# Kernel optimization log

Measured on AMD Instinct MI355X. Metric: run time of the kernel, lower is better.

## Reference

```python
import jax, jax.numpy as jnp
import numpy as np

K = 16  # nsample


def _conv2d(x, w, b=None):
    # 1x1 conv2d: x [B,Cin,K,N], w [Cout,Cin]
    y = jnp.einsum('oc,bckn->bokn', w, x)
    return y if b is None else y + b[None, :, None, None]


def setup_inputs() -> dict:
    key = jax.random.key(0)
    ks = jax.random.split(key, 20)
    B, N1, N2, C = 2, 4096, 8192, 64
    Cin = C + 3  # in_channel + 3
    w = lambda k, shape, fan: (jax.random.normal(k, shape, jnp.float32) / np.sqrt(fan).astype(np.float32))
    return {
        'xyz1': jax.random.normal(ks[0], (B, 3, N1), jnp.float32),
        'xyz2': jax.random.normal(ks[1], (B, 3, N2), jnp.float32),
        'points1': jax.random.normal(ks[2], (B, C, N1), jnp.float32),
        'points2': jax.random.normal(ks[3], (B, C, N2), jnp.float32),
        'w_r0': w(ks[4], (C, Cin), Cin), 'b_r0': jnp.zeros((C,), jnp.float32),
        'w_r1': w(ks[5], (C, C), C), 'b_r1': jnp.zeros((C,), jnp.float32),
        'w_z0': w(ks[6], (C, Cin), Cin), 'b_z0': jnp.zeros((C,), jnp.float32),
        'w_z1': w(ks[7], (C, C), C), 'b_z1': jnp.zeros((C,), jnp.float32),
        'w_h0': w(ks[8], (C, Cin), Cin), 'b_h0': jnp.zeros((C,), jnp.float32),
        'w_h1': w(ks[9], (C, C), C), 'b_h1': jnp.zeros((C,), jnp.float32),
        'w_fuse_r': w(ks[10], (C, C), C),
        'w_fuse_z': w(ks[11], (C, C), C),
        'w_fuse_ro': w(ks[12], (C, C), C),
    }


def reference(xyz1, xyz2, points1, points2,
              w_r0, b_r0, w_r1, b_r1,
              w_z0, b_z0, w_z1, b_z1,
              w_h0, b_h0, w_h1, b_h1,
              w_fuse_r, w_fuse_z, w_fuse_ro):
    x1 = jnp.transpose(xyz1, (0, 2, 1))  # [B,N1,3]
    x2 = jnp.transpose(xyz2, (0, 2, 1))  # [B,N2,3]
    # squared pairwise distances [B,N1,N2]
    sq = (jnp.sum(x1 * x1, -1)[:, :, None]
          + jnp.sum(x2 * x2, -1)[:, None, :]
          - 2.0 * jnp.einsum('bnd,bmd->bnm', x1, x2))
    _, knn = jax.lax.top_k(-sq, K)  # [B,N1,K] smallest distances
    gather = jax.vmap(lambda p, i: p[i])
    nbr_xyz = gather(x2, knn)                 # [B,N1,K,3]
    dir_xyz = nbr_xyz - x1[:, :, None, :]
    p2 = gather(jnp.transpose(points2, (0, 2, 1)), knn)  # [B,N1,K,C]
    new_pts = jnp.transpose(jnp.concatenate([p2, dir_xyz], -1), (0, 3, 2, 1))  # [B,C+3,K,N1]

    lrelu = lambda v: jax.nn.leaky_relu(v, 0.1)
    fuse = lambda w, p: jnp.einsum('oc,bcn->bon', w, p)

    # r gate
    r = _conv2d(new_pts, w_r0, b_r0) + fuse(w_fuse_r, points1)[:, :, None, :]
    r = lrelu(r)
    r = jax.nn.sigmoid(_conv2d(r, w_r1, b_r1))  # [B,C,K,N1]

    # z gate (max over neighbors before last conv)
    z = _conv2d(new_pts, w_z0, b_z0) + fuse(w_fuse_z, points1)[:, :, None, :]
    z = lrelu(z)
    z = jnp.max(z, axis=2, keepdims=True)
    z = jax.nn.sigmoid(_conv2d(z, w_z1, b_z1))[:, :, 0, :]  # [B,C,N1]

    # h candidate
    p1e = _conv2d(r * points1[:, :, None, :], w_fuse_ro)
    h = lrelu(_conv2d(new_pts, w_h0, b_h0) + p1e)
    h = jnp.max(h, axis=2, keepdims=True)
    h = jnp.tanh(_conv2d(h, w_h1, b_h1))[:, :, 0, :]  # [B,C,N1]

    return (1.0 - z) * points1 + z * h
```

## Files before the change

### kernel.cpp

```cpp
#include <hip/hip_runtime.h>
#include <math.h>

typedef __attribute__((ext_vector_type(8))) short bf8_t;
typedef __attribute__((ext_vector_type(4))) float f32x4;

#define NB   2
#define N1S  4096
#define N2S  8192
#define CC   64
#define KK   16
#define GQ   8
#define KTILE 2048

#define M_R0 0
#define M_Z0 1
#define M_H0 2
#define M_R1 3
#define M_Z1 4
#define M_H1 5
#define M_FR 6
#define M_FZ 7
#define M_FRO 8

#define WA_SHORTS   (9*4*2*64*8)
#define WDIR_OFF    (WA_SHORTS*2)
#define WDIR_FLOATS (3*3*64)
#define XP_OFF      (WDIR_OFF + WDIR_FLOATS*4)
#define XP_BYTES    (NB*N2S*16)
#define KIDX_OFF    (XP_OFF + XP_BYTES)
#define KIDX_BYTES  (NB*N1S*KK*4)
#define P2B_OFF     (KIDX_OFF + KIDX_BYTES)
#define P2B_BYTES   ((size_t)NB*N2S*CC*2)

__device__ __forceinline__ float lrelu(float v){ return v > 0.f ? v : 0.1f*v; }
__device__ __forceinline__ float sigm(float v){ return 1.f/(1.f + __expf(-v)); }
__device__ __forceinline__ float tanh_(float v){ return 1.f - 2.f/(__expf(2.f*v) + 1.f); }
__device__ __forceinline__ unsigned short f2bf(float f){
  union { float f; unsigned u; } v; v.f = f;
  unsigned r = v.u + 0x7FFF + ((v.u >> 16) & 1);
  return (unsigned short)(r >> 16);
}

__global__ __launch_bounds__(256) void prep_wA(
    const float* __restrict__ r0, const float* __restrict__ z0, const float* __restrict__ h0,
    const float* __restrict__ r1, const float* __restrict__ z1, const float* __restrict__ h1,
    const float* __restrict__ fr, const float* __restrict__ fz, const float* __restrict__ fro,
    short* __restrict__ wa, float* __restrict__ wdir)
{
  const float* W[9] = {r0, z0, h0, r1, z1, h1, fr, fz, fro};
  const int Ks[9]   = {67, 67, 67, 64, 64, 64, 64, 64, 64};
  const int stride = gridDim.x * 256;
  for (int i = blockIdx.x*256 + threadIdx.x; i < WA_SHORTS; i += stride) {
    const int j = i & 7, l = (i >> 3) & 63, kk = (i >> 9) & 1, r = (i >> 10) & 3, mat = i >> 12;
    const int row = r*16 + (l & 15);
    const int c = kk*32 + ((l >> 4) << 3) + j;
    wa[i] = (short)f2bf(W[mat][row*Ks[mat] + c]);
  }
  for (int i = blockIdx.x*256 + threadIdx.x; i < WDIR_FLOATS; i += stride) {
    const int g = i / 192, rem = i % 192, d = rem / 64, o = rem & 63;
    wdir[i] = W[g][o*67 + 64 + d];
  }
}

__global__ __launch_bounds__(256) void pack_xyz2(const float* __restrict__ xyz2, float4* __restrict__ xp){
  const int i = blockIdx.x*256 + threadIdx.x;
  const int b = i >> 13, j = i & (N2S-1);
  const float x = xyz2[((size_t)(b*3+0))*N2S + j];
  const float y = xyz2[((size_t)(b*3+1))*N2S + j];
  const float z = xyz2[((size_t)(b*3+2))*N2S + j];
  xp[i] = make_float4(x, y, z, (x*x + y*y) + z*z);
}

__global__ __launch_bounds__(256) void transpose_p2(const float* __restrict__ src, unsigned short* __restrict__ dst){
  __shared__ float t[64][65];
  const int b = blockIdx.y; const int j0 = blockIdx.x*64;
  const int tx = threadIdx.x & 63; const int r4 = threadIdx.x >> 6;
  #pragma unroll
  for (int c = r4; c < 64; c += 4) t[c][tx] = src[((size_t)b*CC + c)*N2S + j0 + tx];
  __syncthreads();
  #pragma unroll
  for (int j = r4; j < 64; j += 4) dst[((size_t)b*N2S + j0 + j)*CC + tx] = f2bf(t[tx][j]);
}

__global__ __launch_bounds__(256) void knn_kernel(
    const float* __restrict__ xyz1, const float4* __restrict__ xp, int* __restrict__ idxout)
{
  __shared__ float4 T[KTILE];
  const int tid = threadIdx.x, w = tid >> 6, lane = tid & 63, grp = lane >> 4;
  const int qbase = blockIdx.x*16 + w*4;
  const int b = qbase >> 12;
  const float4* __restrict__ X = xp + (b << 13);
  float qx[4], qy[4], qz[4], s1[4], kth[4], kappa[4], m[4];
  #pragma unroll
  for (int g = 0; g < 4; g++) {
    const int n = (qbase + g) & (N1S-1);
    qx[g] = xyz1[((size_t)(b*3+0))*N1S + n];
    qy[g] = xyz1[((size_t)(b*3+1))*N1S + n];
    qz[g] = xyz1[((size_t)(b*3+2))*N1S + n];
    s1[g] = (qx[g]*qx[g] + qy[g]*qy[g]) + qz[g]*qz[g];
    kth[g] = INFINITY; m[g] = INFINITY;
  }

  #pragma unroll 2
  for (int c0 = 0; c0 < N2S; c0 += 256) {
    const float4 v0 = X[c0 + lane];
    const float4 v1 = X[c0 + 64 + lane];
    const float4 v2 = X[c0 + 128 + lane];
    const float4 v3 = X[c0 + 192 + lane];
    #pragma unroll
    for (int g = 0; g < 4; g++) {
      const float d0 = (s1[g] + v0.w) - 2.f*((qx[g]*v0.x + qy[g]*v0.y) + qz[g]*v0.z);
      const float d1 = (s1[g] + v1.w) - 2.f*((qx[g]*v1.x + qy[g]*v1.y) + qz[g]*v1.z);
      const float d2 = (s1[g] + v2.w) - 2.f*((qx[g]*v2.x + qy[g]*v2.y) + qz[g]*v2.z);
      const float d3 = (s1[g] + v3.w) - 2.f*((qx[g]*v3.x + qy[g]*v3.y) + qz[g]*v3.z);
      m[g] = fminf(m[g], fminf(fminf(d0, d1), fminf(d2, d3)));
    }
  }
  #pragma unroll
  for (int g = 0; g < 4; g++) {
    float v = m[g];
    #pragma unroll
    for (int k = 2; k <= 64; k <<= 1) {
      #pragma unroll
      for (int j = k >> 1; j > 0; j >>= 1) {
        const float pv = __shfl_xor(v, j);
        const bool up = ((lane & k) == 0);
        const bool keepmin = up ? ((lane & j) == 0) : ((lane & j) != 0);
        v = keepmin ? fminf(v, pv) : fmaxf(v, pv);
      }
    }
    kappa[g] = __shfl(v, 16);
  }

  float listd = INFINITY; int listi = 0;
  for (int t0 = 0; t0 < N2S; t0 += KTILE) {
    __syncthreads();
    for (int i = tid; i < KTILE; i += 256) T[i] = X[t0 + i];
    __syncthreads();
    for (int c0 = 0; c0 < KTILE; c0 += 64) {
      const float4 v = T[c0 + lane];
      #pragma unroll
      for (int g = 0; g < 4; g++) {
        const float d = (s1[g] + v.w) - 2.f*((qx[g]*v.x + qy[g]*v.y) + qz[g]*v.z);
        unsigned long long vote = __ballot(d < fminf(kth[g], kappa[g]));
        while (vote) {
          const int src = (int)__builtin_ctzll(vote);
          vote &= vote - 1;
          const float dv = __shfl(d, src);
          if (dv < kth[g]) {
            const int iv = t0 + c0 + src;
            const float ud = __shfl_up(listd, 1);
            const int   ui = __shfl_up(listi, 1);
            const bool ing = (grp == g);
            const bool cm = ing && (dv < listd);
            const bool cp = cm && ((lane & 15) > 0) && (dv < ud);
            listd = cm ? (cp ? ud : dv) : listd;
            listi = cm ? (cp ? ui : iv) : listi;
            kth[g] = __shfl(listd, g*16 + 15);
          }
        }
      }
    }
  }

  {
    bool need = false;
    #pragma unroll
    for (int g = 0; g < 4; g++) need = need || (kth[g] == INFINITY);
    if (__builtin_expect(need, 0)) {
      #pragma unroll
      for (int g = 0; g < 4; g++) {
        if (kth[g] == INFINITY) {
          if (grp == g) { listd = INFINITY; listi = 0; }
          float kk2 = INFINITY;
          for (int c0 = 0; c0 < N2S; c0 += 64) {
            const float4 v = X[c0 + lane];
            const float d = (s1[g] + v.w) - 2.f*((qx[g]*v.x + qy[g]*v.y) + qz[g]*v.z);
            unsigned long long vote = __ballot(d < kk2);
            while (vote) {
              const int src = (int)__builtin_ctzll(vote);
              vote &= vote - 1;
              const float dv = __shfl(d, src);
              if (dv < kk2) {
                const int iv = c0 + src;
                const float ud = __shfl_up(listd, 1);
                const int   ui = __shfl_up(listi, 1);
                const bool ing = (grp == g);
                const bool cm = ing && (dv < listd);
                const bool cp = cm && ((lane & 15) > 0) && (dv < ud);
                listd = cm ? (cp ? ud : dv) : listd;
                listi = cm ? (cp ? ui : iv) : listi;
                kk2 = __shfl(listd, g*16 + 15);
              }
            }
          }
        }
      }
    }
  }
  idxout[(size_t)(qbase + grp)*KK + (lane & 15)] = listi;
}

#define FRAG(mat, kk) (*(const bf8_t*)(wA + (((mat)*4 + w)*2 + (kk))*512 + lane*8))

__global__ __launch_bounds__(256) void gates_kernel(
    const float* __restrict__ xyz1, const float* __restrict__ xyz2,
    const float* __restrict__ points1, const unsigned short* __restrict__ p2b,
    const int* __restrict__ kidx, const short* __restrict__ wA,
    const float* __restrict__ wdir,
    const float* __restrict__ b_r0, const float* __restrict__ b_z0,
    const float* __restrict__ b_h0, const float* __restrict__ b_r1,
    const float* __restrict__ b_z1, const float* __restrict__ b_h1,
    float* __restrict__ out)
{
  __shared__ __align__(16) short featB[2][GQ][64][8];
  __shared__ __align__(16) short rB[2][GQ][64][8];
  __shared__ __align__(16) float p1f[64][GQ];
  __shared__ __align__(16) short p1B[2][64][8];
  __shared__ float BFr[64][GQ], BFz[64][GQ];
  __shared__ float zmaxL[64][GQ], hmaxL[64][GQ];
  __shared__ float biasL[6][64];
  __shared__ float dirL[3][GQ*KK];
  __shared__ __align__(16) float obuf[64][GQ];

  const int tid = threadIdx.x;
  const int w = tid >> 6, lane = tid & 63;
  const int b  = blockIdx.x >> 9;
  const int n0 = (blockIdx.x & 511) * GQ;
  const int cq = lane & 15;
  const int reg_o0 = w*16 + ((lane >> 4) << 2);
  const f32x4 zero4 = {0.f, 0.f, 0.f, 0.f};

  for (int i = tid; i < 6*64; i += 256) {
    const int a = i >> 6, o = i & 63;
    const float* bp = (a==0)?b_r0:(a==1)?b_z0:(a==2)?b_h0:(a==3)?b_r1:(a==4)?b_z1:b_h1;
    biasL[a][o] = bp[o];
  }
  if (tid < 64) {
    const float* sp = points1 + ((size_t)(b*CC + tid))*N1S + n0;
    *(float4*)&p1f[tid][0] = ((const float4*)sp)[0];
    *(float4*)&p1f[tid][4] = ((const float4*)sp)[1];
  }
  ((unsigned long long*)&p1B[0][0][0])[tid] = 0ULL;
  if (tid < 128) {
    const int m = tid, qg = n0 + (m >> 4);
    const int j = kidx[(size_t)((b << 12) + qg)*KK + (m & 15)];
    #pragma unroll
    for (int d = 0; d < 3; d++)
      dirL[d][m] = xyz2[((size_t)(b*3+d))*N2S + j] - xyz1[((size_t)(b*3+d))*N1S + qg];
  }
  {
    const int m = tid >> 1, half = tid & 1;
    const int ct = m >> 4;
    const int qg = n0 + ct;
    const int j = kidx[(size_t)((b << 12) + qg)*KK + (m & 15)];
    const uint4* __restrict__ src = (const uint4*)(p2b + (((size_t)(b << 13) + j)*CC + half*32));
    #pragma unroll
    for (int gi = 0; gi < 4; gi++)
      *(uint4*)&featB[half][ct][gi*16 + (m & 15)][0] = src[gi];
  }
  __syncthreads();

  {
    const int s0 = tid*4;
    const int j0 = s0 & 7, l = (s0 >> 3) & 63, kk = s0 >> 9;
    const int q = l & 15;
    if (q < 8) {
      unsigned short t0[4];
      #pragma unroll
      for (int jj = 0; jj < 4; jj++)
        t0[jj] = f2bf(p1f[kk*32 + ((l >> 4) << 3) + j0 + jj][q]);
      uint2 pk; pk.x = t0[0] | ((unsigned)t0[1] << 16); pk.y = t0[2] | ((unsigned)t0[3] << 16);
      *(uint2*)&p1B[kk][l][j0] = pk;
    }
  }
  __syncthreads();

  {
    const bf8_t fa0 = FRAG(M_FR, 0), fa1 = FRAG(M_FR, 1);
    const bf8_t ga0 = FRAG(M_FZ, 0), ga1 = FRAG(M_FZ, 1);
    const bf8_t pb0 = *(const bf8_t*)&p1B[0][lane][0];
    const bf8_t pb1 = *(const bf8_t*)&p1B[1][lane][0];
    f32x4 ar = __builtin_amdgcn_mfma_f32_16x16x32_bf16(fa0, pb0, zero4, 0, 0, 0);
    ar = __builtin_amdgcn_mfma_f32_16x16x32_bf16(fa1, pb1, ar, 0, 0, 0);
    f32x4 az = __builtin_amdgcn_mfma_f32_16x16x32_bf16(ga0, pb0, zero4, 0, 0, 0);
    az = __builtin_amdgcn_mfma_f32_16x16x32_bf16(ga1, pb1, az, 0, 0, 0);
    if (cq < 8) {
      #pragma unroll
      for (int r2 = 0; r2 < 4; r2++) {
        const int o = reg_o0 + r2;
        BFr[o][cq] = ar[r2] + biasL[0][o];
        BFz[o][cq] = az[r2] + biasL[1][o];
      }
    }
  }

  {
    const bf8_t ra0 = FRAG(M_R0, 0), ra1 = FRAG(M_R0, 1);
    const bf8_t za0 = FRAG(M_Z0, 0), za1 = FRAG(M_Z0, 1);
    float wdr[3][4], wdz[3][4];
    #pragma unroll
    for (int d = 0; d < 3; d++)
      #pragma unroll
      for (int r2 = 0; r2 < 4; r2++) {
        wdr[d][r2] = wdir[(0*3 + d)*64 + reg_o0 + r2];
        wdz[d][r2] = wdir[(1*3 + d)*64 + reg_o0 + r2];
      }
    const int kkv = reg_o0 >> 5, lp = ((reg_o0 & 31) >> 3)*16 + cq, j0 = reg_o0 & 7;
    #pragma unroll
    for (int ct = 0; ct < GQ; ct++) {
      const bf8_t fb0 = *(const bf8_t*)&featB[0][ct][lane][0];
      const bf8_t fb1 = *(const bf8_t*)&featB[1][ct][lane][0];
      f32x4 accr = __builtin_amdgcn_mfma_f32_16x16x32_bf16(ra0, fb0, zero4, 0, 0, 0);
      accr = __builtin_amdgcn_mfma_f32_16x16x32_bf16(ra1, fb1, accr, 0, 0, 0);
      f32x4 accz = __builtin_amdgcn_mfma_f32_16x16x32_bf16(za0, fb0, zero4, 0, 0, 0);
      accz = __builtin_amdgcn_mfma_f32_16x16x32_bf16(za1, fb1, accz, 0, 0, 0);
      const int m = ct*16 + cq;
      const float d0 = dirL[0][m], d1 = dirL[1][m], d2 = dirL[2][m];
      unsigned short rpk[4]; float zv[4];
      #pragma unroll
      for (int r2 = 0; r2 < 4; r2++) {
        const int o = reg_o0 + r2;
        float rv = accr[r2] + BFr[o][ct] + wdr[0][r2]*d0 + wdr[1][r2]*d1 + wdr[2][r2]*d2;
        rpk[r2] = f2bf(lrelu(rv));
        float zt = accz[r2] + BFz[o][ct] + wdz[0][r2]*d0 + wdz[1][r2]*d1 + wdz[2][r2]*d2;
        zv[r2] = lrelu(zt);
      }
      uint2 pk; pk.x = rpk[0] | ((unsigned)rpk[1] << 16); pk.y = rpk[2] | ((unsigned)rpk[3] << 16);
      *(uint2*)&rB[kkv][ct][lp][j0] = pk;
      #pragma unroll
      for (int r2 = 0; r2 < 4; r2++) {
        float vv = zv[r2];
        vv = fmaxf(vv, __shfl_xor(vv, 1));
        vv = fmaxf(vv, __shfl_xor(vv, 2));
        vv = fmaxf(vv, __shfl_xor(vv, 4));
        vv = fmaxf(vv, __shfl_xor(vv, 8));
        zv[r2] = vv;
      }
      if (cq == 0) {
        #pragma unroll
        for (int r2 = 0; r2 < 4; r2++) zmaxL[reg_o0 + r2][ct] = zv[r2];
      }
    }
  }
  __syncthreads();

  uint2 rpK[GQ];
  float zg[4];
  {
    const bf8_t r1a0 = FRAG(M_R1, 0), r1a1 = FRAG(M_R1, 1);
    #pragma unroll
    for (int ct = 0; ct < GQ; ct++) {
      const bf8_t b0 = *(const bf8_t*)&rB[0][ct][lane][0];
      const bf8_t b1 = *(const bf8_t*)&rB[1][ct][lane][0];
      f32x4 acc = __builtin_amdgcn_mfma_f32_16x16x32_bf16(r1a0, b0, zero4, 0, 0, 0);
      acc = __builtin_amdgcn_mfma_f32_16x16x32_bf16(r1a1, b1, acc, 0, 0, 0);
      unsigned short pk4[4];
      #pragma unroll
      for (int r2 = 0; r2 < 4; r2++) {
        const int o = reg_o0 + r2;
        const float rg = sigm(acc[r2] + biasL[3][o]);
        pk4[r2] = f2bf(rg * p1f[o][ct]);
      }
      rpK[ct].x = pk4[0] | ((unsigned)pk4[1] << 16);
      rpK[ct].y = pk4[2] | ((unsigned)pk4[3] << 16);
    }
    const bf8_t z1a0 = FRAG(M_Z1, 0), z1a1 = FRAG(M_Z1, 1);
    const int qc = cq < 8 ? cq : 7;
    bf8_t zb0, zb1;
    #pragma unroll
    for (int j = 0; j < 8; j++) {
      zb0[j] = (short)f2bf(zmaxL[((lane >> 4) << 3) + j][qc]);
      zb1[j] = (short)f2bf(zmaxL[32 + ((lane >> 4) << 3) + j][qc]);
    }
    f32x4 az = __builtin_amdgcn_mfma_f32_16x16x32_bf16(z1a0, zb0, zero4, 0, 0, 0);
    az = __builtin_amdgcn_mfma_f32_16x16x32_bf16(z1a1, zb1, az, 0, 0, 0);
    #pragma unroll
    for (int r2 = 0; r2 < 4; r2++) zg[r2] = sigm(az[r2] + biasL[4][reg_o0 + r2]);
  }
  __syncthreads();

  {
    const int kkv = reg_o0 >> 5, lp = ((reg_o0 & 31) >> 3)*16 + cq, j0 = reg_o0 & 7;
    #pragma unroll
    for (int ct = 0; ct < GQ; ct++) *(uint2*)&rB[kkv][ct][lp][j0] = rpK[ct];
  }
  __syncthreads();

  {
    const bf8_t h0a0 = FRAG(M_H0, 0), h0a1 = FRAG(M_H0, 1);
    const bf8_t foa0 = FRAG(M_FRO, 0), foa1 = FRAG(M_FRO, 1);
    float wdh[3][4];
    #pragma unroll
    for (int d = 0; d < 3; d++)
      #pragma unroll
      for (int r2 = 0; r2 < 4; r2++) wdh[d][r2] = wdir[(2*3 + d)*64 + reg_o0 + r2];
    #pragma unroll
    for (int ct = 0; ct < GQ; ct++) {
      const bf8_t fb0 = *(const bf8_t*)&featB[0][ct][lane][0];
      const bf8_t fb1 = *(const bf8_t*)&featB[1][ct][lane][0];
      const bf8_t rb0 = *(const bf8_t*)&rB[0][ct][lane][0];
      const bf8_t rb1 = *(const bf8_t*)&rB[1][ct][lane][0];
      f32x4 acc = __builtin_amdgcn_mfma_f32_16x16x32_bf16(h0a0, fb0, zero4, 0, 0, 0);
      acc = __builtin_amdgcn_mfma_f32_16x16x32_bf16(h0a1, fb1, acc, 0, 0, 0);
      acc = __builtin_amdgcn_mfma_f32_16x16x32_bf16(foa0, rb0, acc, 0, 0, 0);
      acc = __builtin_amdgcn_mfma_f32_16x16x32_bf16(foa1, rb1, acc, 0, 0, 0);
      const int m = ct*16 + cq;
      const float d0 = dirL[0][m], d1 = dirL[1][m], d2 = dirL[2][m];
      float hv[4];
      #pragma unroll
      for (int r2 = 0; r2 < 4; r2++) {
        const int o = reg_o0 + r2;
        hv[r2] = lrelu(acc[r2] + biasL[2][o] + wdh[0][r2]*d0 + wdh[1][r2]*d1 + wdh[2][r2]*d2);
      }
      #pragma unroll
      for (int r2 = 0; r2 < 4; r2++) {
        float vv = hv[r2];
        vv = fmaxf(vv, __shfl_xor(vv, 1));
        vv = fmaxf(vv, __shfl_xor(vv, 2));
        vv = fmaxf(vv, __shfl_xor(vv, 4));
        vv = fmaxf(vv, __shfl_xor(vv, 8));
        hv[r2] = vv;
      }
      if (cq == 0) {
        #pragma unroll
        for (int r2 = 0; r2 < 4; r2++) hmaxL[reg_o0 + r2][ct] = hv[r2];
      }
    }
  }
  __syncthreads();

  {
    const bf8_t h1a0 = FRAG(M_H1, 0), h1a1 = FRAG(M_H1, 1);
    const int qc = cq < 8 ? cq : 7;
    bf8_t hb0, hb1;
    #pragma unroll
    for (int j = 0; j < 8; j++) {
      hb0[j] = (short)f2bf(hmaxL[((lane >> 4) << 3) + j][qc]);
      hb1[j] = (short)f2bf(hmaxL[32 + ((lane >> 4) << 3) + j][qc]);
    }
    f32x4 ah = __builtin_amdgcn_mfma_f32_16x16x32_bf16(h1a0, hb0, zero4, 0, 0, 0);
    ah = __builtin_amdgcn_mfma_f32_16x16x32_bf16(h1a1, hb1, ah, 0, 0, 0);
    if (cq < 8) {
      #pragma unroll
      for (int r2 = 0; r2 < 4; r2++) {
        const int o = reg_o0 + r2;
        const float hg = tanh_(ah[r2] + biasL[5][o]);
        obuf[o][cq] = (1.f - zg[r2])*p1f[o][cq] + zg[r2]*hg;
      }
    }
  }
  __syncthreads();
  if (tid < 128) {
    const int c = tid >> 1, q4 = (tid & 1)*4;
    *(float4*)(out + ((size_t)(b*CC + c))*N1S + n0 + q4) = *(float4*)&obuf[c][q4];
  }
}

extern "C" void kernel_launch(void* const* d_in, const int* in_sizes, int n_in,
                              void* d_out, int out_size, void* d_ws, size_t ws_size,
                              hipStream_t stream) {
  const float* xyz1    = (const float*)d_in[0];
  const float* xyz2    = (const float*)d_in[1];
  const float* points1 = (const float*)d_in[2];
  const float* points2 = (const float*)d_in[3];
  const float* w_r0 = (const float*)d_in[4];
  const float* b_r0 = (const float*)d_in[5];
  const float* w_r1 = (const float*)d_in[6];
  const float* b_r1 = (const float*)d_in[7];
  const float* w_z0 = (const float*)d_in[8];
  const float* b_z0 = (const float*)d_in[9];
  const float* w_z1 = (const float*)d_in[10];
  const float* b_z1 = (const float*)d_in[11];
  const float* w_h0 = (const float*)d_in[12];
  const float* b_h0 = (const float*)d_in[13];
  const float* w_h1 = (const float*)d_in[14];
  const float* b_h1 = (const float*)d_in[15];
  const float* w_fr  = (const float*)d_in[16];
  const float* w_fz  = (const float*)d_in[17];
  const float* w_fro = (const float*)d_in[18];
  float* out = (float*)d_out;

  short*  wa   = (short*)d_ws;
  float*  wdir = (float*)((char*)d_ws + WDIR_OFF);
  float4* xp   = (float4*)((char*)d_ws + XP_OFF);
  int*    kidx = (int*)((char*)d_ws + KIDX_OFF);
  unsigned short* p2b = (unsigned short*)((char*)d_ws + P2B_OFF);

  prep_wA<<<16, 256, 0, stream>>>(w_r0, w_z0, w_h0, w_r1, w_z1, w_h1,
                                  w_fr, w_fz, w_fro, wa, wdir);
  pack_xyz2<<<64, 256, 0, stream>>>(xyz2, xp);
  transpose_p2<<<dim3(N2S/64, NB), dim3(256), 0, stream>>>(points2, p2b);

  knn_kernel<<<512, 256, 0, stream>>>(xyz1, xp, kidx);

  gates_kernel<<<1024, 256, 0, stream>>>(
      xyz1, xyz2, points1, p2b, kidx, wa, wdir,
      b_r0, b_z0, b_h0, b_r1, b_z1, b_h1, out);
}
```

Baseline: 202.8 us.

## Split KNN candidate scan across two waves per query and merge lists

The KNN kernel now gives each wave 2 queries instead of 4 and splits the 8192 candidates into two halves handled by paired waves. The per-half top-16 lists are merged through shared memory with a bitonic sort that breaks ties by index. The LDS tile staging of candidates is dropped, and the scan reads global memory directly. This quadruples the block count to raise parallelism and occupancy, and shortens the serial per-wave scan. In exchange it adds a merge step and pays for twice the kappa prefilter work over the halves.

Measured after the change: 199.2 us. No clear change (-1.8%).

```diff
diff --git a/kernel.cpp b/kernel.cpp
--- a/kernel.cpp
+++ b/kernel.cpp
@@ -10,7 +10,6 @@
 #define CC   64
 #define KK   16
 #define GQ   8
-#define KTILE 2048
 
 #define M_R0 0
 #define M_Z0 1
@@ -85,15 +84,19 @@
 __global__ __launch_bounds__(256) void knn_kernel(
     const float* __restrict__ xyz1, const float4* __restrict__ xp, int* __restrict__ idxout)
 {
-  __shared__ float4 T[KTILE];
+  __shared__ float pdL[4][2][16];
+  __shared__ int   piL[4][2][16];
   const int tid = threadIdx.x, w = tid >> 6, lane = tid & 63, grp = lane >> 4;
-  const int qbase = blockIdx.x*16 + w*4;
+  const int qbase = blockIdx.x*4;
   const int b = qbase >> 12;
+  const int q0 = qbase + (w >> 1)*2;
+  const int half = w & 1;
+  const int hbase = half*(N2S/2);
   const float4* __restrict__ X = xp + (b << 13);
-  float qx[4], qy[4], qz[4], s1[4], kth[4], kappa[4], m[4];
+  float qx[2], qy[2], qz[2], s1[2], kth[2], kappa[2], m[2];
   #pragma unroll
-  for (int g = 0; g < 4; g++) {
-    const int n = (qbase + g) & (N1S-1);
+  for (int g = 0; g < 2; g++) {
+    const int n = (q0 + g) & (N1S-1);
     qx[g] = xyz1[((size_t)(b*3+0))*N1S + n];
     qy[g] = xyz1[((size_t)(b*3+1))*N1S + n];
     qz[g] = xyz1[((size_t)(b*3+2))*N1S + n];
@@ -102,13 +105,13 @@
   }
 
   #pragma unroll 2
-  for (int c0 = 0; c0 < N2S; c0 += 256) {
-    const float4 v0 = X[c0 + lane];
-    const float4 v1 = X[c0 + 64 + lane];
-    const float4 v2 = X[c0 + 128 + lane];
-    const float4 v3 = X[c0 + 192 + lane];
-    #pragma unroll
-    for (int g = 0; g < 4; g++) {
+  for (int c0 = 0; c0 < N2S/2; c0 += 256) {
+    const float4 v0 = X[hbase + c0 + lane];
+    const float4 v1 = X[hbase + c0 + 64 + lane];
+    const float4 v2 = X[hbase + c0 + 128 + lane];
+    const float4 v3 = X[hbase + c0 + 192 + lane];
+    #pragma unroll
+    for (int g = 0; g < 2; g++) {
       const float d0 = (s1[g] + v0.w) - 2.f*((qx[g]*v0.x + qy[g]*v0.y) + qz[g]*v0.z);
       const float d1 = (s1[g] + v1.w) - 2.f*((qx[g]*v1.x + qy[g]*v1.y) + qz[g]*v1.z);
       const float d2 = (s1[g] + v2.w) - 2.f*((qx[g]*v2.x + qy[g]*v2.y) + qz[g]*v2.z);
@@ -117,7 +120,7 @@
     }
   }
   #pragma unroll
-  for (int g = 0; g < 4; g++) {
+  for (int g = 0; g < 2; g++) {
     float v = m[g];
     #pragma unroll
     for (int k = 2; k <= 64; k <<= 1) {
@@ -133,31 +136,27 @@
   }
 
   float listd = INFINITY; int listi = 0;
-  for (int t0 = 0; t0 < N2S; t0 += KTILE) {
-    __syncthreads();
-    for (int i = tid; i < KTILE; i += 256) T[i] = X[t0 + i];
-    __syncthreads();
-    for (int c0 = 0; c0 < KTILE; c0 += 64) {
-      const float4 v = T[c0 + lane];
-      #pragma unroll
-      for (int g = 0; g < 4; g++) {
-        const float d = (s1[g] + v.w) - 2.f*((qx[g]*v.x + qy[g]*v.y) + qz[g]*v.z);
-        unsigned long long vote = __ballot(d < fminf(kth[g], kappa[g]));
-        while (vote) {
-          const int src = (int)__builtin_ctzll(vote);
-          vote &= vote - 1;
-          const float dv = __shfl(d, src);
-          if (dv < kth[g]) {
-            const int iv = t0 + c0 + src;
-            const float ud = __shfl_up(listd, 1);
-            const int   ui = __shfl_up(listi, 1);
-            const bool ing = (grp == g);
-            const bool cm = ing && (dv < listd);
-            const bool cp = cm && ((lane & 15) > 0) && (dv < ud);
-            listd = cm ? (cp ? ud : dv) : listd;
-            listi = cm ? (cp ? ui : iv) : listi;
-            kth[g] = __shfl(listd, g*16 + 15);
-          }
+  #pragma unroll 2
+  for (int c0 = 0; c0 < N2S/2; c0 += 64) {
+    const float4 v = X[hbase + c0 + lane];
+    #pragma unroll
+    for (int g = 0; g < 2; g++) {
+      const float d = (s1[g] + v.w) - 2.f*((qx[g]*v.x + qy[g]*v.y) + qz[g]*v.z);
+      unsigned long long vote = __ballot(d < fminf(kth[g], kappa[g]));
+      while (vote) {
+        const int src = (int)__builtin_ctzll(vote);
+        vote &= vote - 1;
+        const float dv = __shfl(d, src);
+        if (dv < kth[g]) {
+          const int iv = hbase + c0 + src;
+          const float ud = __shfl_up(listd, 1);
+          const int   ui = __shfl_up(listi, 1);
+          const bool ing = (grp == g);
+          const bool cm = ing && (dv < listd);
+          const bool cp = cm && ((lane & 15) > 0) && (dv < ud);
+          listd = cm ? (cp ? ud : dv) : listd;
+          listi = cm ? (cp ? ui : iv) : listi;
+          kth[g] = __shfl(listd, g*16 + 15);
         }
       }
     }
@@ -166,15 +165,15 @@
   {
     bool need = false;
     #pragma unroll
-    for (int g = 0; g < 4; g++) need = need || (kth[g] == INFINITY);
+    for (int g = 0; g < 2; g++) need = need || (kth[g] == INFINITY);
     if (__builtin_expect(need, 0)) {
       #pragma unroll
-      for (int g = 0; g < 4; g++) {
+      for (int g = 0; g < 2; g++) {
         if (kth[g] == INFINITY) {
           if (grp == g) { listd = INFINITY; listi = 0; }
           float kk2 = INFINITY;
-          for (int c0 = 0; c0 < N2S; c0 += 64) {
-            const float4 v = X[c0 + lane];
+          for (int c0 = 0; c0 < N2S/2; c0 += 64) {
+            const float4 v = X[hbase + c0 + lane];
             const float d = (s1[g] + v.w) - 2.f*((qx[g]*v.x + qy[g]*v.y) + qz[g]*v.z);
             unsigned long long vote = __ballot(d < kk2);
             while (vote) {
@@ -182,7 +181,7 @@
               vote &= vote - 1;
               const float dv = __shfl(d, src);
               if (dv < kk2) {
-                const int iv = c0 + src;
+                const int iv = hbase + c0 + src;
                 const float ud = __shfl_up(listd, 1);
                 const int   ui = __shfl_up(listi, 1);
                 const bool ing = (grp == g);
@@ -198,7 +197,32 @@
       }
     }
   }
-  idxout[(size_t)(qbase + grp)*KK + (lane & 15)] = listi;
+
+  if (grp < 2) {
+    const int qi = (w >> 1)*2 + grp;
+    pdL[qi][half][lane & 15] = listd;
+    piL[qi][half][lane & 15] = listi;
+  }
+  __syncthreads();
+
+  {
+    float d = (lane < 32) ? pdL[w][lane >> 4][lane & 15] : INFINITY;
+    int   i = (lane < 32) ? piL[w][lane >> 4][lane & 15] : 0x7fffffff;
+    #pragma unroll
+    for (int k = 2; k <= 64; k <<= 1) {
+      #pragma unroll
+      for (int j = k >> 1; j > 0; j >>= 1) {
+        const float pdv = __shfl_xor(d, j);
+        const int   piv = __shfl_xor(i, j);
+        const bool keepmin = (((lane & k) == 0) == ((lane & j) == 0));
+        const bool ownless = (d < pdv) || (d == pdv && i < piv);
+        const bool takeown = keepmin ? ownless : !ownless;
+        d = takeown ? d : pdv;
+        i = takeown ? i : piv;
+      }
+    }
+    if (lane < KK) idxout[(size_t)(qbase + w)*KK + lane] = i;
+  }
 }
 
 #define FRAG(mat, kk) (*(const bf8_t*)(wA + (((mat)*4 + w)*2 + (kk))*512 + lane*8))
@@ -492,7 +516,7 @@
   pack_xyz2<<<64, 256, 0, stream>>>(xyz2, xp);
   transpose_p2<<<dim3(N2S/64, NB), dim3(256), 0, stream>>>(points2, p2b);
 
-  knn_kernel<<<512, 256, 0, stream>>>(xyz1, xp, kidx);
+  knn_kernel<<<2048, 256, 0, stream>>>(xyz1, xp, kidx);
 
   gates_kernel<<<1024, 256, 0, stream>>>(
       xyz1, xyz2, points1, p2b, kidx, wa, wdir,
```
